# Optimization experiments

Hardware: AMD Instinct MI355X
Metric: run time of the kernel (lower is better)

Reference implementation:

```python
import jax, jax.numpy as jnp
import numpy as np

EPS = 1e-12  # matches tf.nn.l2_normalize epsilon used by K.l2_normalize


def _l2_normalize(v):
    # normalize along last axis
    sq = jnp.sum(v * v, axis=-1, keepdims=True)
    return v * jax.lax.rsqrt(jnp.maximum(sq, EPS))


def setup_inputs() -> dict:
    key = jax.random.key(0)
    k1, k2, k3 = jax.random.split(key, 3)
    B, L1, L2, D, P = 64, 200, 200, 300, 16
    sent1 = jax.random.normal(k1, (B, L1, D), dtype=jnp.float32)
    sent2 = jax.random.normal(k2, (B, L2, D), dtype=jnp.float32)
    kernel = jax.random.normal(k3, (P, D), dtype=jnp.float32) * 0.1
    return {"sent1": sent1, "sent2": sent2, "kernel": kernel}


def reference(sent1, sent2, kernel):
    # per-perspective weighted vectors: (B, L, P, D)
    v1 = _l2_normalize(sent1[:, :, None, :] * kernel)
    v2 = _l2_normalize(sent2[:, :, None, :] * kernel)
    # cosine similarity matrix per perspective: (B, L1, L2, P)
    sim = jnp.einsum('bipd,bjpd->bijp', v1, v2)
    # max over second sequence axis -> (B, L1, P)
    return jnp.max(sim, axis=2)
```

## Files before the change

### kernel.cpp

```cpp
#include <hip/hip_runtime.h>
#include <math.h>

#define BBATCH 64
#define LL 200
#define DD 300
#define PP 16
#define EPSV 1e-12f
#define KG 320
#define PS 328
#define NCH 10
#define SRS 324

typedef _Float16 f16x8 __attribute__((ext_vector_type(8)));
typedef float f32x4v __attribute__((ext_vector_type(4)));

__global__ __launch_bounds__(256) void prep_kernel(const float* __restrict__ s1,
                                                   const float* __restrict__ s2,
                                                   const float* __restrict__ kern,
                                                   float* __restrict__ n1inv,
                                                   _Float16* __restrict__ n2inv,
                                                   _Float16* __restrict__ h1,
                                                   _Float16* __restrict__ h2,
                                                   _Float16* __restrict__ ksqt) {
    const int grp   = blockIdx.x;
    const int which = blockIdx.y;
    const int b     = blockIdx.z;
    const float* s  = which ? s2 : s1;
    _Float16* hout  = which ? h2 : h1;
    const int r0    = grp * 32;
    const int t     = threadIdx.x;

    __shared__ float    sr[32][SRS];
    __shared__ _Float16 kqf[640 * 8];

    for (int idx = t; idx < 32 * 75; idx += 256) {
        int r = idx / 75, c4 = (idx - r * 75) * 4;
        int row = r0 + r;
        float4 v = make_float4(0.f, 0.f, 0.f, 0.f);
        if (row < LL) v = *(const float4*)&s[((size_t)b * LL + row) * DD + c4];
        *(float4*)&sr[r][c4] = v;
    }
    for (int idx = t; idx < 32 * 24; idx += 256) {
        int r = idx / 24, cc = 300 + (idx - r * 24);
        sr[r][cc] = 0.f;
    }
    for (int ent = t; ent < 640; ent += 256) {
        int ch = ent >> 6, rem = ent & 63;
        int quad = rem >> 4, p = rem & 15;
        int k0 = ch * 32 + quad * 8;
        f16x8 h;
        if (k0 + 8 <= DD) {
            float4 a = *(const float4*)&kern[p * DD + k0];
            float4 d = *(const float4*)&kern[p * DD + k0 + 4];
            h[0] = (_Float16)(a.x * a.x); h[1] = (_Float16)(a.y * a.y);
            h[2] = (_Float16)(a.z * a.z); h[3] = (_Float16)(a.w * a.w);
            h[4] = (_Float16)(d.x * d.x); h[5] = (_Float16)(d.y * d.y);
            h[6] = (_Float16)(d.z * d.z); h[7] = (_Float16)(d.w * d.w);
        } else {
#pragma unroll
            for (int e = 0; e < 8; e++) {
                float kv = (k0 + e < DD) ? kern[p * DD + k0 + e] : 0.f;
                h[e] = (_Float16)(kv * kv);
            }
        }
        *(f16x8*)&kqf[ent * 8] = h;
    }
    __syncthreads();

    const int lane = t & 63;
    const int w    = t >> 6;

    if (w < 2) {
        const int rg   = w;
        const int c    = lane & 15;
        const int quad = lane >> 4;
        f32x4v nacc = (f32x4v)0.f;
#pragma unroll
        for (int ch = 0; ch < NCH; ch++) {
            float4 a = *(const float4*)&sr[rg * 16 + c][ch * 32 + quad * 8];
            float4 d = *(const float4*)&sr[rg * 16 + c][ch * 32 + quad * 8 + 4];
            f16x8 sa;
            sa[0] = (_Float16)(a.x * a.x); sa[1] = (_Float16)(a.y * a.y);
            sa[2] = (_Float16)(a.z * a.z); sa[3] = (_Float16)(a.w * a.w);
            sa[4] = (_Float16)(d.x * d.x); sa[5] = (_Float16)(d.y * d.y);
            sa[6] = (_Float16)(d.z * d.z); sa[7] = (_Float16)(d.w * d.w);
            f16x8 bk = *(const f16x8*)&kqf[((ch * 4 + quad) * 16 + c) * 8];
            nacc = __builtin_amdgcn_mfma_f32_16x16x32_f16(sa, bk, nacc, 0, 0, 0);
        }
#pragma unroll
        for (int r = 0; r < 4; r++) {
            int row = r0 + rg * 16 + quad * 4 + r;
            if (row < LL) {
                float inv = 1.0f / sqrtf(fmaxf(nacc[r], EPSV));
                if (which) n2inv[((size_t)b * LL + row) * PP + c] = (_Float16)inv;
                else       n1inv[((size_t)b * LL + row) * PP + c] = inv;
            }
        }
    } else {
        const int base = (w - 2) * 640;
        for (int u = base + lane; u < base + 640; u += 64) {
            int r = u / 40, e0 = (u - r * 40) * 8;
            int row = r0 + r;
            if (row < LL) {
                float4 a = *(const float4*)&sr[r][e0];
                float4 d = *(const float4*)&sr[r][e0 + 4];
                f16x8 h;
                h[0] = (_Float16)a.x; h[1] = (_Float16)a.y; h[2] = (_Float16)a.z; h[3] = (_Float16)a.w;
                h[4] = (_Float16)d.x; h[5] = (_Float16)d.y; h[6] = (_Float16)d.z; h[7] = (_Float16)d.w;
                *(f16x8*)&hout[((size_t)b * LL + row) * KG + e0] = h;
            }
        }
    }

    if (which == 1 && grp == 6 && b == 0) {
        for (int ent = t; ent < 640; ent += 256)
            *(f16x8*)&ksqt[(size_t)ent * 8] = *(const f16x8*)&kqf[ent * 8];
    }
}

__global__ __launch_bounds__(256, 1) void maxsim_kernel(const _Float16* __restrict__ h1,
                                                        const _Float16* __restrict__ h2,
                                                        const _Float16* __restrict__ ksqt,
                                                        const _Float16* __restrict__ n2inv,
                                                        const float* __restrict__ n1inv,
                                                        float* __restrict__ out) {
    extern __shared__ __align__(16) char smem[];
    _Float16* h2s = (_Float16*)smem;
    _Float16* n2s = h2s + 200 * PS;
    _Float16* kqs = n2s + 200 * PP;

    const int blk  = blockIdx.x;
    const int b    = blk & 63;
    const int v    = blk >> 6;
    const int iblk = v & 1;
    const int pgrp = v >> 1;
    const int i0   = iblk ? 72 : 0;
    const int t    = threadIdx.x;

    const int lane = t & 63;
    const int w    = t >> 6;
    const int c    = lane & 15;
    const int quad = lane >> 4;
    const int ibase = i0 + w * 32;

    f16x8 af[2][NCH];
    {
        const _Float16* g1 = h1 + (size_t)b * LL * KG;
#pragma unroll
        for (int it = 0; it < 2; it++)
#pragma unroll
            for (int ch = 0; ch < NCH; ch++)
                af[it][ch] = *(const f16x8*)&g1[(size_t)(ibase + it * 16 + c) * KG + ch * 32 + quad * 8];
    }

    {
        const _Float16* g2 = h2 + (size_t)b * LL * KG;
        for (int idx = t; idx < 200 * 40; idx += 256) {
            int r = idx / 40, q = idx - r * 40;
            *(f16x8*)&h2s[r * PS + q * 8] = *(const f16x8*)&g2[(size_t)idx * 8];
        }
        const _Float16* gn = n2inv + (size_t)b * LL * PP;
        for (int idx = t; idx < 400; idx += 256)
            *(f16x8*)&n2s[idx * 8] = *(const f16x8*)&gn[(size_t)idx * 8];
        for (int idx = t; idx < 640; idx += 256)
            *(f16x8*)&kqs[idx * 8] = *(const f16x8*)&ksqt[(size_t)idx * 8];
    }
    __syncthreads();

    for (int pp = 0; pp < 4; pp++) {
        const int p0 = pgrp * 8 + pp * 2;
        float rmax[2][2][4];
#pragma unroll
        for (int pq = 0; pq < 2; pq++)
#pragma unroll
            for (int it = 0; it < 2; it++)
#pragma unroll
                for (int r = 0; r < 4; r++) rmax[pq][it][r] = -INFINITY;

#pragma unroll 1
        for (int pass = 0; pass < 6; pass++) {
            const int jb0 = pass * 32;
            const int jb1 = jb0 + 16;
            f32x4v acc[2][2][2];
#pragma unroll
            for (int pq = 0; pq < 2; pq++)
#pragma unroll
                for (int it = 0; it < 2; it++)
#pragma unroll
                    for (int jt = 0; jt < 2; jt++) acc[pq][it][jt] = (f32x4v)0.f;

            f16x8 kq0 = *(const f16x8*)&kqs[quad * 128 + p0 * 8];
            f16x8 kq1 = *(const f16x8*)&kqs[quad * 128 + p0 * 8 + 8];
            f16x8 hb0 = *(const f16x8*)&h2s[(jb0 + c) * PS + quad * 8];
            f16x8 hb1 = *(const f16x8*)&h2s[(jb1 + c) * PS + quad * 8];

#pragma unroll
            for (int ch = 0; ch < NCH; ch++) {
                f16x8 kq0n = kq0, kq1n = kq1, hb0n = hb0, hb1n = hb1;
                if (ch < NCH - 1) {
                    kq0n = *(const f16x8*)&kqs[(ch + 1) * 512 + quad * 128 + p0 * 8];
                    kq1n = *(const f16x8*)&kqs[(ch + 1) * 512 + quad * 128 + p0 * 8 + 8];
                    hb0n = *(const f16x8*)&h2s[(jb0 + c) * PS + (ch + 1) * 32 + quad * 8];
                    hb1n = *(const f16x8*)&h2s[(jb1 + c) * PS + (ch + 1) * 32 + quad * 8];
                }
                f16x8 sa00 = af[0][ch] * kq0;
                f16x8 sa10 = af[1][ch] * kq0;
                f16x8 sa01 = af[0][ch] * kq1;
                f16x8 sa11 = af[1][ch] * kq1;
                acc[0][0][0] = __builtin_amdgcn_mfma_f32_16x16x32_f16(sa00, hb0, acc[0][0][0], 0, 0, 0);
                acc[0][1][0] = __builtin_amdgcn_mfma_f32_16x16x32_f16(sa10, hb0, acc[0][1][0], 0, 0, 0);
                acc[1][0][0] = __builtin_amdgcn_mfma_f32_16x16x32_f16(sa01, hb0, acc[1][0][0], 0, 0, 0);
                acc[1][1][0] = __builtin_amdgcn_mfma_f32_16x16x32_f16(sa11, hb0, acc[1][1][0], 0, 0, 0);
                acc[0][0][1] = __builtin_amdgcn_mfma_f32_16x16x32_f16(sa00, hb1, acc[0][0][1], 0, 0, 0);
                acc[0][1][1] = __builtin_amdgcn_mfma_f32_16x16x32_f16(sa10, hb1, acc[0][1][1], 0, 0, 0);
                acc[1][0][1] = __builtin_amdgcn_mfma_f32_16x16x32_f16(sa01, hb1, acc[1][0][1], 0, 0, 0);
                acc[1][1][1] = __builtin_amdgcn_mfma_f32_16x16x32_f16(sa11, hb1, acc[1][1][1], 0, 0, 0);
                kq0 = kq0n; kq1 = kq1n; hb0 = hb0n; hb1 = hb1n;
            }
#pragma unroll
            for (int pq = 0; pq < 2; pq++) {
                float n20 = (float)n2s[(jb0 + c) * PP + p0 + pq];
                float n21 = (float)n2s[(jb1 + c) * PP + p0 + pq];
#pragma unroll
                for (int it = 0; it < 2; it++)
#pragma unroll
                    for (int r = 0; r < 4; r++) {
                        rmax[pq][it][r] = fmaxf(rmax[pq][it][r], acc[pq][it][0][r] * n20);
                        rmax[pq][it][r] = fmaxf(rmax[pq][it][r], acc[pq][it][1][r] * n21);
                    }
            }
        }

        {
            const int jb0 = 184;
            f32x4v acc[2][2];
#pragma unroll
            for (int pq = 0; pq < 2; pq++)
#pragma unroll
                for (int it = 0; it < 2; it++) acc[pq][it] = (f32x4v)0.f;

            f16x8 kq0 = *(const f16x8*)&kqs[quad * 128 + p0 * 8];
            f16x8 kq1 = *(const f16x8*)&kqs[quad * 128 + p0 * 8 + 8];
            f16x8 hb0 = *(const f16x8*)&h2s[(jb0 + c) * PS + quad * 8];

#pragma unroll
            for (int ch = 0; ch < NCH; ch++) {
                f16x8 kq0n = kq0, kq1n = kq1, hb0n = hb0;
                if (ch < NCH - 1) {
                    kq0n = *(const f16x8*)&kqs[(ch + 1) * 512 + quad * 128 + p0 * 8];
                    kq1n = *(const f16x8*)&kqs[(ch + 1) * 512 + quad * 128 + p0 * 8 + 8];
                    hb0n = *(const f16x8*)&h2s[(jb0 + c) * PS + (ch + 1) * 32 + quad * 8];
                }
                f16x8 sa00 = af[0][ch] * kq0;
                f16x8 sa10 = af[1][ch] * kq0;
                f16x8 sa01 = af[0][ch] * kq1;
                f16x8 sa11 = af[1][ch] * kq1;
                acc[0][0] = __builtin_amdgcn_mfma_f32_16x16x32_f16(sa00, hb0, acc[0][0], 0, 0, 0);
                acc[0][1] = __builtin_amdgcn_mfma_f32_16x16x32_f16(sa10, hb0, acc[0][1], 0, 0, 0);
                acc[1][0] = __builtin_amdgcn_mfma_f32_16x16x32_f16(sa01, hb0, acc[1][0], 0, 0, 0);
                acc[1][1] = __builtin_amdgcn_mfma_f32_16x16x32_f16(sa11, hb0, acc[1][1], 0, 0, 0);
                kq0 = kq0n; kq1 = kq1n; hb0 = hb0n;
            }
#pragma unroll
            for (int pq = 0; pq < 2; pq++) {
                float n20 = (float)n2s[(jb0 + c) * PP + p0 + pq];
#pragma unroll
                for (int it = 0; it < 2; it++)
#pragma unroll
                    for (int r = 0; r < 4; r++)
                        rmax[pq][it][r] = fmaxf(rmax[pq][it][r], acc[pq][it][r] * n20);
            }
        }

#pragma unroll
        for (int pq = 0; pq < 2; pq++) {
#pragma unroll
            for (int m = 1; m <= 8; m <<= 1)
#pragma unroll
                for (int it = 0; it < 2; it++)
#pragma unroll
                    for (int r = 0; r < 4; r++)
                        rmax[pq][it][r] = fmaxf(rmax[pq][it][r], __shfl_xor(rmax[pq][it][r], m));
            if (c == 0) {
#pragma unroll
                for (int it = 0; it < 2; it++)
#pragma unroll
                    for (int r = 0; r < 4; r++) {
                        int i = ibase + it * 16 + quad * 4 + r;
                        size_t o = ((size_t)b * LL + i) * PP + p0 + pq;
                        out[o] = rmax[pq][it][r] * n1inv[o];
                    }
            }
        }
    }
}

extern "C" void kernel_launch(void* const* d_in, const int* in_sizes, int n_in,
                              void* d_out, int out_size, void* d_ws, size_t ws_size,
                              hipStream_t stream) {
    const float* sent1  = (const float*)d_in[0];
    const float* sent2  = (const float*)d_in[1];
    const float* kernel = (const float*)d_in[2];
    float* out = (float*)d_out;

    char* ws = (char*)d_ws;
    float*    n1inv = (float*)ws;                  ws += (size_t)BBATCH * LL * PP * 4;
    _Float16* n2inv = (_Float16*)ws;               ws += (size_t)BBATCH * LL * PP * 2;
    _Float16* h1    = (_Float16*)ws;               ws += (size_t)BBATCH * LL * KG * 2;
    _Float16* h2    = (_Float16*)ws;               ws += (size_t)BBATCH * LL * KG * 2;
    _Float16* ksqt  = (_Float16*)ws;

    prep_kernel<<<dim3(7, 2, BBATCH), 256, 0, stream>>>(sent1, sent2, kernel,
                                                        n1inv, n2inv, h1, h2, ksqt);

    const int lds_bytes = (200 * PS + 200 * PP + 5120) * 2;
    hipFuncSetAttribute((const void*)maxsim_kernel,
                        hipFuncAttributeMaxDynamicSharedMemorySize, lds_bytes);
    maxsim_kernel<<<dim3(256, 1, 1), 256, lds_bytes, stream>>>(h1, h2, ksqt, n2inv, n1inv, out);
}
```

Before: 127.1 us.

## Split squared-kernel prep into its own kernel and drop LDS staging in prep

Moves the computation of squared fp16 kernel weights into a separate one-block kernel, so each prep block no longer rebuilds them. The prep kernel now converts sentence rows straight from global memory to fp16 without LDS staging, then re-reads its own fp16 output from global to compute norms with MFMA, squaring in fp16. This cuts LDS use and redundant work per block, at the cost of an extra launch, a global read-back after a block-level barrier, and squaring after fp16 rounding, which changes precision slightly.

```diff
diff --git a/kernel.cpp b/kernel.cpp
--- a/kernel.cpp
+++ b/kernel.cpp
@@ -9,19 +9,45 @@
 #define KG 320
 #define PS 328
 #define NCH 10
-#define SRS 324
 
 typedef _Float16 f16x8 __attribute__((ext_vector_type(8)));
 typedef float f32x4v __attribute__((ext_vector_type(4)));
 
+__global__ __launch_bounds__(256) void ksq_kernel(const float* __restrict__ kern,
+                                                  _Float16* __restrict__ ksqt) {
+    __shared__ float kl[16][320];
+    const int t = threadIdx.x;
+    for (int idx = t; idx < 16 * 75; idx += 256) {
+        int p = idx / 75, c4 = (idx - p * 75) * 4;
+        *(float4*)&kl[p][c4] = *(const float4*)&kern[p * DD + c4];
+    }
+    for (int idx = t; idx < 16 * 20; idx += 256) {
+        int p = idx / 20, cc = 300 + (idx - p * 20);
+        kl[p][cc] = 0.f;
+    }
+    __syncthreads();
+    for (int ent = t; ent < 640; ent += 256) {
+        int ch = ent >> 6, rem = ent & 63;
+        int quad = rem >> 4, p = rem & 15;
+        int k0 = ch * 32 + quad * 8;
+        float4 a = *(const float4*)&kl[p][k0];
+        float4 d = *(const float4*)&kl[p][k0 + 4];
+        f16x8 h;
+        h[0] = (_Float16)(a.x * a.x); h[1] = (_Float16)(a.y * a.y);
+        h[2] = (_Float16)(a.z * a.z); h[3] = (_Float16)(a.w * a.w);
+        h[4] = (_Float16)(d.x * d.x); h[5] = (_Float16)(d.y * d.y);
+        h[6] = (_Float16)(d.z * d.z); h[7] = (_Float16)(d.w * d.w);
+        *(f16x8*)&ksqt[(size_t)ent * 8] = h;
+    }
+}
+
 __global__ __launch_bounds__(256) void prep_kernel(const float* __restrict__ s1,
                                                    const float* __restrict__ s2,
-                                                   const float* __restrict__ kern,
                                                    float* __restrict__ n1inv,
                                                    _Float16* __restrict__ n2inv,
                                                    _Float16* __restrict__ h1,
                                                    _Float16* __restrict__ h2,
-                                                   _Float16* __restrict__ ksqt) {
+                                                   const _Float16* __restrict__ ksqt) {
     const int grp   = blockIdx.x;
     const int which = blockIdx.y;
     const int b     = blockIdx.z;
@@ -30,61 +56,45 @@
     const int r0    = grp * 32;
     const int t     = threadIdx.x;
 
-    __shared__ float    sr[32][SRS];
-    __shared__ _Float16 kqf[640 * 8];
-
-    for (int idx = t; idx < 32 * 75; idx += 256) {
-        int r = idx / 75, c4 = (idx - r * 75) * 4;
+    for (int idx = t; idx < 32 * 40; idx += 256) {
+        int r = idx / 40, q = idx - r * 40;
         int row = r0 + r;
-        float4 v = make_float4(0.f, 0.f, 0.f, 0.f);
-        if (row < LL) v = *(const float4*)&s[((size_t)b * LL + row) * DD + c4];
-        *(float4*)&sr[r][c4] = v;
-    }
-    for (int idx = t; idx < 32 * 24; idx += 256) {
-        int r = idx / 24, cc = 300 + (idx - r * 24);
-        sr[r][cc] = 0.f;
-    }
-    for (int ent = t; ent < 640; ent += 256) {
-        int ch = ent >> 6, rem = ent & 63;
-        int quad = rem >> 4, p = rem & 15;
-        int k0 = ch * 32 + quad * 8;
+        if (row >= LL) continue;
+        int q8 = q * 8;
+        const float* src = &s[((size_t)b * LL + row) * DD];
         f16x8 h;
-        if (k0 + 8 <= DD) {
-            float4 a = *(const float4*)&kern[p * DD + k0];
-            float4 d = *(const float4*)&kern[p * DD + k0 + 4];
-            h[0] = (_Float16)(a.x * a.x); h[1] = (_Float16)(a.y * a.y);
-            h[2] = (_Float16)(a.z * a.z); h[3] = (_Float16)(a.w * a.w);
-            h[4] = (_Float16)(d.x * d.x); h[5] = (_Float16)(d.y * d.y);
-            h[6] = (_Float16)(d.z * d.z); h[7] = (_Float16)(d.w * d.w);
+        if (q8 + 8 <= DD) {
+            float4 a = *(const float4*)&src[q8];
+            float4 d = *(const float4*)&src[q8 + 4];
+            h[0] = (_Float16)a.x; h[1] = (_Float16)a.y; h[2] = (_Float16)a.z; h[3] = (_Float16)a.w;
+            h[4] = (_Float16)d.x; h[5] = (_Float16)d.y; h[6] = (_Float16)d.z; h[7] = (_Float16)d.w;
+        } else if (q8 < DD) {
+            float4 a = *(const float4*)&src[q8];
+            h[0] = (_Float16)a.x; h[1] = (_Float16)a.y; h[2] = (_Float16)a.z; h[3] = (_Float16)a.w;
+            h[4] = (_Float16)0.f; h[5] = (_Float16)0.f; h[6] = (_Float16)0.f; h[7] = (_Float16)0.f;
         } else {
 #pragma unroll
-            for (int e = 0; e < 8; e++) {
-                float kv = (k0 + e < DD) ? kern[p * DD + k0 + e] : 0.f;
-                h[e] = (_Float16)(kv * kv);
-            }
-        }
-        *(f16x8*)&kqf[ent * 8] = h;
+            for (int e = 0; e < 8; e++) h[e] = (_Float16)0.f;
+        }
+        *(f16x8*)&hout[((size_t)b * LL + row) * KG + q8] = h;
     }
     __syncthreads();
 
     const int lane = t & 63;
     const int w    = t >> 6;
-
     if (w < 2) {
         const int rg   = w;
         const int c    = lane & 15;
         const int quad = lane >> 4;
+        int arow = r0 + rg * 16 + c;
+        int rowc = arow < LL ? arow : LL - 1;
+        const _Float16* hb = &hout[((size_t)b * LL + rowc) * KG];
         f32x4v nacc = (f32x4v)0.f;
 #pragma unroll
         for (int ch = 0; ch < NCH; ch++) {
-            float4 a = *(const float4*)&sr[rg * 16 + c][ch * 32 + quad * 8];
-            float4 d = *(const float4*)&sr[rg * 16 + c][ch * 32 + quad * 8 + 4];
-            f16x8 sa;
-            sa[0] = (_Float16)(a.x * a.x); sa[1] = (_Float16)(a.y * a.y);
-            sa[2] = (_Float16)(a.z * a.z); sa[3] = (_Float16)(a.w * a.w);
-            sa[4] = (_Float16)(d.x * d.x); sa[5] = (_Float16)(d.y * d.y);
-            sa[6] = (_Float16)(d.z * d.z); sa[7] = (_Float16)(d.w * d.w);
-            f16x8 bk = *(const f16x8*)&kqf[((ch * 4 + quad) * 16 + c) * 8];
+            f16x8 av = *(const f16x8*)&hb[ch * 32 + quad * 8];
+            f16x8 sa = av * av;
+            f16x8 bk = *(const f16x8*)&ksqt[((size_t)(ch * 4 + quad) * 16 + c) * 8];
             nacc = __builtin_amdgcn_mfma_f32_16x16x32_f16(sa, bk, nacc, 0, 0, 0);
         }
 #pragma unroll
@@ -96,25 +106,6 @@
                 else       n1inv[((size_t)b * LL + row) * PP + c] = inv;
             }
         }
-    } else {
-        const int base = (w - 2) * 640;
-        for (int u = base + lane; u < base + 640; u += 64) {
-            int r = u / 40, e0 = (u - r * 40) * 8;
-            int row = r0 + r;
-            if (row < LL) {
-                float4 a = *(const float4*)&sr[r][e0];
-                float4 d = *(const float4*)&sr[r][e0 + 4];
-                f16x8 h;
-                h[0] = (_Float16)a.x; h[1] = (_Float16)a.y; h[2] = (_Float16)a.z; h[3] = (_Float16)a.w;
-                h[4] = (_Float16)d.x; h[5] = (_Float16)d.y; h[6] = (_Float16)d.z; h[7] = (_Float16)d.w;
-                *(f16x8*)&hout[((size_t)b * LL + row) * KG + e0] = h;
-            }
-        }
-    }
-
-    if (which == 1 && grp == 6 && b == 0) {
-        for (int ent = t; ent < 640; ent += 256)
-            *(f16x8*)&ksqt[(size_t)ent * 8] = *(const f16x8*)&kqf[ent * 8];
     }
 }
 
@@ -310,7 +301,9 @@
     _Float16* h2    = (_Float16*)ws;               ws += (size_t)BBATCH * LL * KG * 2;
     _Float16* ksqt  = (_Float16*)ws;
 
-    prep_kernel<<<dim3(7, 2, BBATCH), 256, 0, stream>>>(sent1, sent2, kernel,
+    ksq_kernel<<<1, 256, 0, stream>>>(kernel, ksqt);
+
+    prep_kernel<<<dim3(7, 2, BBATCH), 256, 0, stream>>>(sent1, sent2,
                                                         n1inv, n2inv, h1, h2, ksqt);
 
     const int lds_bytes = (200 * PS + 200 * PP + 5120) * 2;
```

Measured after the change: 128.3 us. No clear change (+0.9%).
